# Kernel tuning notes

Measured on AMD Instinct MI355X. Metric: run time of the kernel, lower is better.

## Reference

```python
import jax, jax.numpy as jnp
import numpy as np

NUM_CODEBOOKS = 8
CODEBOOK_SIZE = 4096
SUBVEC_DIM = 128
NUM_CLASSES = 1000
BATCH = 8192
INPUT_DIM = NUM_CODEBOOKS * SUBVEC_DIM


def setup_inputs() -> dict:
    key = jax.random.key(0)
    k1, k2, k3 = jax.random.split(key, 3)
    x = jax.random.normal(k1, (BATCH, INPUT_DIM), dtype=jnp.float32)
    codebooks = jax.random.normal(k2, (NUM_CODEBOOKS, CODEBOOK_SIZE, SUBVEC_DIM), dtype=jnp.float32)
    tables = jax.random.normal(k3, (NUM_CODEBOOKS, CODEBOOK_SIZE, NUM_CLASSES), dtype=jnp.float32)
    return {"x": x, "codebooks": codebooks, "tables": tables}


def reference(x, codebooks, tables):
    B = x.shape[0]
    # [B, nc, d] subvectors
    xr = x.reshape(B, NUM_CODEBOOKS, SUBVEC_DIM)
    # (||x||^2 term is constant per (b, codebook) so it does not affect argmin)
    dots = jnp.einsum('bkd,kcd->bkc', xr, codebooks)            # [B, nc, K]
    c_sq = jnp.sum(codebooks * codebooks, axis=-1)              # [nc, K]
    dists = c_sq[None, :, :] - 2.0 * dots                        # [B, nc, K]
    indices = jnp.argmin(dists, axis=-1)                         # [B, nc] int
    # Gather per-codebook class score rows and sum over codebooks.
    # tables: [nc, K, C]; indices: [B, nc]
    gathered = jnp.take_along_axis(
        tables[None, :, :, :],                                   # [1, nc, K, C]
        indices[:, :, None, None],                               # [B, nc, 1, 1]
        axis=2,
    )                                                            # [B, nc, 1, C]
    scores = jnp.sum(gathered[:, :, 0, :], axis=1)               # [B, C]
    return scores
```

## Files before the change

kernel.cpp:

```cpp
#include <hip/hip_runtime.h>
#include <stdint.h>

#define NC   8
#define NK   4096
#define DD   128
#define NCLS 1000
#define NB   8192

#define CSQ_F32   4194304
#define P_U32     4300000
#define TAIL_LO   4300
#define TAIL_HI   4366

typedef _Float16 f16;
typedef f16   f16x8 __attribute__((ext_vector_type(8)));
typedef float f32x4 __attribute__((ext_vector_type(4)));

typedef const __attribute__((address_space(1))) unsigned int g_u32;
typedef __attribute__((address_space(3))) unsigned int l_u32;

__device__ __forceinline__ void gll16(const char* g, char* l) {
    __builtin_amdgcn_global_load_lds((g_u32*)g, (l_u32*)l, 16, 0, 0);
}

__device__ __forceinline__ int swz(int row, int kg) {
    return (row * 256 + kg * 16) ^ ((row & 7) << 4);
}

__device__ __forceinline__ void ins(float cv, int ci, float& v1, int& i1,
                                    float& v2, int& i2) {
    const bool b1 = (cv > v1) || (cv == v1 && ci < i1);
    const bool b2 = (cv > v2) || (cv == v2 && ci < i2);
    if (b1) { v2 = v1; i2 = i1; v1 = cv; i1 = ci; }
    else if (b2) { v2 = cv; i2 = ci; }
}

__device__ __forceinline__ void cvt8(const float4 v0, const float4 v1,
                                     f16x8& h, f16x8& l) {
    float vs[8] = {v0.x, v0.y, v0.z, v0.w, v1.x, v1.y, v1.z, v1.w};
#pragma unroll
    for (int i = 0; i < 8; ++i) {
        const float v = vs[i];
        const f16 hi = (f16)v;
        h[i] = hi;
        l[i] = (f16)((v - (float)hi) * 2048.0f);
    }
}

__global__ __launch_bounds__(256) void prep_cb(const float* __restrict__ cb,
                                               char* __restrict__ bimg,
                                               float* __restrict__ csq) {
    const int chunk = blockIdx.x, k = blockIdx.y, t = threadIdx.x;
    const float* src = cb + ((size_t)k * NK + (size_t)chunk * 64) * DD;
    char* dst = bimg + (size_t)(k * 64 + chunk) * 32768;
#pragma unroll
    for (int j = 0; j < 4; ++j) {
        const int col = j * 16 + (t >> 4);
        const int kg  = t & 15;
        const float* p = src + (size_t)col * DD + kg * 8;
        const float4 v0 = *(const float4*)p;
        const float4 v1 = *(const float4*)(p + 4);
        float vs[8] = {v0.x, v0.y, v0.z, v0.w, v1.x, v1.y, v1.z, v1.w};
        f16x8 h, l;
        float ss = 0.f;
#pragma unroll
        for (int i = 0; i < 8; ++i) {
            const float v = vs[i];
            ss += v * v;
            const f16 hi = (f16)v;
            h[i] = hi;
            l[i] = (f16)((v - (float)hi) * 2048.0f);
        }
#pragma unroll
        for (int m = 1; m < 16; m <<= 1) ss += __shfl_xor(ss, m, 16);
        if (kg == 0) csq[k * NK + chunk * 64 + col] = ss;
        const int r = col & 31;
        const int half = col >> 5;
        const int off = half * 8192 + swz(r, kg);
        *(f16x8*)(dst + off)         = h;
        *(f16x8*)(dst + 16384 + off) = l;
    }
}

template <int W, bool ISS>
__device__ __forceinline__ void chunk_step(
    int c, int& bcur, int& bnx, char* lds, const char* gB,
    int w, int lane, int l15,
    const f16x8 (&Ah)[4], const f16x8 (&Al)[4], const int (&boff)[4][2],
    float (&rv1)[4], float (&rv2)[4], int (&ri1)[4], int (&ri2)[4]) {

    asm volatile("s_waitcnt vmcnt(%0)" :: "i"(W) : "memory");
    __builtin_amdgcn_s_barrier();

    if (ISS) {
        const int cn = c + 2;
        const char* src = gB + (size_t)(cn >> 1) * 32768 + (size_t)(cn & 1) * 8192;
        char* dstb = lds + bnx * 16384 + w * 1024;
        gll16(src + w * 1024 + lane * 16, dstb);
        gll16(src + 16384 + w * 1024 + lane * 16, dstb + 8192);
    }

    char* bufc = lds + bcur * 16384;
    const float cs0 = *(const float*)(lds + 49152 + (c * 32 + l15) * 4);
    const float cs1 = *(const float*)(lds + 49152 + (c * 32 + 16 + l15) * 4);
    f32x4 a10 = (f32x4){-0.5f * cs0, -0.5f * cs0, -0.5f * cs0, -0.5f * cs0};
    f32x4 a11 = (f32x4){-0.5f * cs1, -0.5f * cs1, -0.5f * cs1, -0.5f * cs1};
    f32x4 a20 = (f32x4){0.f, 0.f, 0.f, 0.f};
    f32x4 a21 = (f32x4){0.f, 0.f, 0.f, 0.f};

    __builtin_amdgcn_s_setprio(1);
#pragma unroll
    for (int kk = 0; kk < 4; ++kk) {
        const f16x8 bh0 = *(const f16x8*)(bufc + boff[kk][0]);
        const f16x8 bh1 = *(const f16x8*)(bufc + boff[kk][1]);
        const f16x8 bl0 = *(const f16x8*)(bufc + 8192 + boff[kk][0]);
        const f16x8 bl1 = *(const f16x8*)(bufc + 8192 + boff[kk][1]);
        a10 = __builtin_amdgcn_mfma_f32_16x16x32_f16(Ah[kk], bh0, a10, 0, 0, 0);
        a11 = __builtin_amdgcn_mfma_f32_16x16x32_f16(Ah[kk], bh1, a11, 0, 0, 0);
        a20 = __builtin_amdgcn_mfma_f32_16x16x32_f16(Ah[kk], bl0, a20, 0, 0, 0);
        a21 = __builtin_amdgcn_mfma_f32_16x16x32_f16(Ah[kk], bl1, a21, 0, 0, 0);
        a20 = __builtin_amdgcn_mfma_f32_16x16x32_f16(Al[kk], bh0, a20, 0, 0, 0);
        a21 = __builtin_amdgcn_mfma_f32_16x16x32_f16(Al[kk], bh1, a21, 0, 0, 0);
    }
    __builtin_amdgcn_s_setprio(0);

    const int col0 = c * 32 + l15;
#pragma unroll
    for (int q = 0; q < 4; ++q) {
        const float s0 = fmaf(a20[q], 4.8828125e-4f, a10[q]);
        const float s1 = fmaf(a21[q], 4.8828125e-4f, a11[q]);
        float cv; int ci;
        if (s1 > s0) { cv = s1; ci = col0 + 16; }
        else         { cv = s0; ci = col0; }
        if (cv > rv1[q]) {
            rv2[q] = rv1[q]; ri2[q] = ri1[q];
            rv1[q] = cv;     ri1[q] = ci;
        } else if (cv > rv2[q]) {
            rv2[q] = cv; ri2[q] = ci;
        }
    }
    bcur = (bcur == 2) ? 0 : bcur + 1;
    bnx  = (bnx  == 2) ? 0 : bnx  + 1;
}

__global__ __launch_bounds__(512, 4) void gemm_argmin(
    const float* __restrict__ x, const char* __restrict__ bimg,
    const float* __restrict__ csq_g, uint32_t* __restrict__ pk) {
    __shared__ char lds[65536];
    const int t = threadIdx.x;
    const int lane = t & 63, w = t >> 6;
    const int bm = blockIdx.x, k = blockIdx.y;
    const int l15 = lane & 15, l4 = lane >> 4;

    {
        const float4* cg = (const float4*)(csq_g + k * NK);
        float4* cl = (float4*)(lds + 49152);
        cl[t] = cg[t];
        cl[t + 512] = cg[t + 512];
    }

    f16x8 Ah[4], Al[4];
    {
        const float* xrow = x + (size_t)(bm * 128 + w * 16 + l15) * 1024 + k * DD;
#pragma unroll
        for (int kk = 0; kk < 4; ++kk) {
            const float* p = xrow + (kk * 4 + l4) * 8;
            cvt8(*(const float4*)p, *(const float4*)(p + 4), Ah[kk], Al[kk]);
        }
    }

    int boff[4][2];
#pragma unroll
    for (int kk = 0; kk < 4; ++kk) {
#pragma unroll
        for (int n = 0; n < 2; ++n)
            boff[kk][n] = swz(n * 16 + l15, kk * 4 + l4);
    }

    float rv1[4], rv2[4];
    int   ri1[4], ri2[4];
#pragma unroll
    for (int q = 0; q < 4; ++q) {
        rv1[q] = -3.402823466e38f; rv2[q] = -3.402823466e38f;
        ri1[q] = 0; ri2[q] = 0;
    }

    __syncthreads();

    const char* gB = bimg + (size_t)k * 64 * 32768;
#pragma unroll
    for (int cn = 0; cn < 2; ++cn) {
        const char* src = gB + (size_t)(cn >> 1) * 32768 + (size_t)(cn & 1) * 8192;
        char* dstb = lds + cn * 16384 + w * 1024;
        gll16(src + w * 1024 + lane * 16, dstb);
        gll16(src + 16384 + w * 1024 + lane * 16, dstb + 8192);
    }

    int bcur = 0, bnx = 2;
#pragma unroll 1
    for (int c = 0; c < 126; ++c)
        chunk_step<2, true>(c, bcur, bnx, lds, gB, w, lane, l15,
                            Ah, Al, boff, rv1, rv2, ri1, ri2);
    chunk_step<2, false>(126, bcur, bnx, lds, gB, w, lane, l15,
                         Ah, Al, boff, rv1, rv2, ri1, ri2);
    chunk_step<0, false>(127, bcur, bnx, lds, gB, w, lane, l15,
                         Ah, Al, boff, rv1, rv2, ri1, ri2);

#pragma unroll
    for (int m = 1; m < 16; m <<= 1) {
#pragma unroll
        for (int q = 0; q < 4; ++q) {
            const float ov1 = __shfl_xor(rv1[q], m, 16);
            const int   oi1 = __shfl_xor(ri1[q], m, 16);
            const float ov2 = __shfl_xor(rv2[q], m, 16);
            const int   oi2 = __shfl_xor(ri2[q], m, 16);
            ins(ov1, oi1, rv1[q], ri1[q], rv2[q], ri2[q]);
            ins(ov2, oi2, rv1[q], ri1[q], rv2[q], ri2[q]);
        }
    }
    if (l15 == 0) {
#pragma unroll
        for (int q = 0; q < 4; ++q) {
            const int row = bm * 128 + w * 16 + l4 * 4 + q;
            pk[(size_t)row * NC + k] =
                (uint32_t)ri1[q] | ((uint32_t)ri2[q] << 16);
        }
    }
}

__global__ __launch_bounds__(512) void reloc_main(const uint32_t* __restrict__ pk,
                                                  uint32_t* __restrict__ hdr) {
    const int g = blockIdx.x * 512 + threadIdx.x;
    const int b = g >> 3, k = g & 7;
    const uint32_t v = pk[g];
    if (b < TAIL_LO || b >= TAIL_HI) hdr[(size_t)b * NCLS + k] = v;
}

__global__ __launch_bounds__(256) void reloc_tail(const uint32_t* __restrict__ pk,
                                                  uint32_t* __restrict__ hdr) {
    for (int g = threadIdx.x; g < (TAIL_HI - TAIL_LO) * 8; g += 256) {
        const int b = TAIL_LO + (g >> 3), k = g & 7;
        hdr[(size_t)b * NCLS + k] = pk[(size_t)b * 8 + k];
    }
}

__global__ __launch_bounds__(256) void finish(const float* __restrict__ x,
                                              const float* __restrict__ cb,
                                              const float* __restrict__ tables,
                                              float* __restrict__ out) {
    const int b = blockIdx.x, t = threadIdx.x;
    const int lane = t & 63, w = t >> 6;
    __shared__ uint32_t hdr_s[8];
    __shared__ int rows_s[8];
    if (t < 8) hdr_s[t] = ((const uint32_t*)out)[(size_t)b * NCLS + t];
    __syncthreads();
#pragma unroll
    for (int kq = 0; kq < 2; ++kq) {
        const int k = w * 2 + kq;
        const uint32_t h = hdr_s[k];
        const int i1 = (int)(h & 0xFFFFu), i2 = (int)(h >> 16);
        const float x0 = x[(size_t)b * 1024 + k * 128 + lane];
        const float x1 = x[(size_t)b * 1024 + k * 128 + 64 + lane];
        const float* c1p = cb + ((size_t)k * NK + i1) * DD;
        const float* c2p = cb + ((size_t)k * NK + i2) * DD;
        const float c10 = c1p[lane], c11 = c1p[64 + lane];
        const float c20 = c2p[lane], c21 = c2p[64 + lane];
        double d1 = (double)c10 * c10 - 2.0 * (double)x0 * c10
                  + (double)c11 * c11 - 2.0 * (double)x1 * c11;
        double d2 = (double)c20 * c20 - 2.0 * (double)x0 * c20
                  + (double)c21 * c21 - 2.0 * (double)x1 * c21;
#pragma unroll
        for (int m = 32; m >= 1; m >>= 1) {
            d1 += __shfl_xor(d1, m, 64);
            d2 += __shfl_xor(d2, m, 64);
        }
        if (lane == 0)
            rows_s[k] = (d1 < d2) ? i1 : (d2 < d1 ? i2 : (i1 < i2 ? i1 : i2));
    }
    __syncthreads();
    if (t < 250) {
        float4 acc = {0.f, 0.f, 0.f, 0.f};
#pragma unroll
        for (int k = 0; k < NC; ++k) {
            const float4 v =
                *((const float4*)(tables + ((size_t)k * NK + rows_s[k]) * NCLS) + t);
            acc.x += v.x; acc.y += v.y; acc.z += v.z; acc.w += v.w;
        }
        *((float4*)(out + (size_t)b * NCLS) + t) = acc;
    }
}

extern "C" void kernel_launch(void* const* d_in, const int* in_sizes, int n_in,
                              void* d_out, int out_size, void* d_ws, size_t ws_size,
                              hipStream_t stream) {
    const float* x      = (const float*)d_in[0];
    const float* cb     = (const float*)d_in[1];
    const float* tables = (const float*)d_in[2];
    float* out = (float*)d_out;

    char*     bimg = (char*)d_out;
    float*    csq  = (float*)d_out + CSQ_F32;
    uint32_t* pk   = (uint32_t*)d_out + P_U32;
    uint32_t* hdr  = (uint32_t*)d_out;

    prep_cb<<<dim3(64, NC), 256, 0, stream>>>(cb, bimg, csq);
    gemm_argmin<<<dim3(64, NC), 512, 0, stream>>>(x, bimg, csq, pk);
    reloc_main<<<128, 512, 0, stream>>>(pk, hdr);
    reloc_tail<<<1, 256, 0, stream>>>(pk, hdr);
    finish<<<NB, 256, 0, stream>>>(x, cb, tables, out);
}
```

Measured before the change: 483.6 us.

## Drop codebook low-half split, keep top-3 candidates with exact rescoring

The codebook is now stored only as a single fp16 image, and only the x operand keeps its hi/lo split. This cuts the MFMAs per chunk from six to four and halves the LDS and global traffic for B. To make up for the lost precision, the argmin pass keeps three candidates instead of two, and the finish kernel rescores all three in double precision. The layout is also simplified: -0.5*csq is precomputed, the block order is interleaved across codebooks, and the reloc step becomes one kernel using a fixed stash cutoff. The risk is that fp16 rounding of the codebook pushes the true argmin out of the top three for some rows.

```diff
diff --git a/kernel.cpp b/kernel.cpp
--- a/kernel.cpp
+++ b/kernel.cpp
@@ -7,10 +7,10 @@
 #define NCLS 1000
 #define NB   8192
 
-#define CSQ_F32   4194304
-#define P_U32     4300000
-#define TAIL_LO   4300
-#define TAIL_HI   4366
+#define BIMG_B   0
+#define CSQ_B    8388608
+#define STASH_B  8519680
+#define BCUT     2176
 
 typedef _Float16 f16;
 typedef f16   f16x8 __attribute__((ext_vector_type(8)));
@@ -27,12 +27,22 @@
     return (row * 256 + kg * 16) ^ ((row & 7) << 4);
 }
 
-__device__ __forceinline__ void ins(float cv, int ci, float& v1, int& i1,
-                                    float& v2, int& i2) {
-    const bool b1 = (cv > v1) || (cv == v1 && ci < i1);
-    const bool b2 = (cv > v2) || (cv == v2 && ci < i2);
-    if (b1) { v2 = v1; i2 = i1; v1 = cv; i1 = ci; }
-    else if (b2) { v2 = cv; i2 = ci; }
+__device__ __forceinline__ void ins3(float cv, int ci,
+                                     float& v1, int& i1, float& v2, int& i2,
+                                     float& v3, int& i3) {
+    if (cv > v1) { v3 = v2; i3 = i2; v2 = v1; i2 = i1; v1 = cv; i1 = ci; }
+    else if (cv > v2) { v3 = v2; i3 = i2; v2 = cv; i2 = ci; }
+    else if (cv > v3) { v3 = cv; i3 = ci; }
+}
+__device__ __forceinline__ void ins3t(float cv, int ci,
+                                      float& v1, int& i1, float& v2, int& i2,
+                                      float& v3, int& i3) {
+    const bool g1 = (cv > v1) || (cv == v1 && ci < i1);
+    const bool g2 = (cv > v2) || (cv == v2 && ci < i2);
+    const bool g3 = (cv > v3) || (cv == v3 && ci < i3);
+    if (g1) { v3 = v2; i3 = i2; v2 = v1; i2 = i1; v1 = cv; i1 = ci; }
+    else if (g2) { v3 = v2; i3 = i2; v2 = cv; i2 = ci; }
+    else if (g3) { v3 = cv; i3 = ci; }
 }
 
 __device__ __forceinline__ void cvt8(const float4 v0, const float4 v1,
@@ -48,37 +58,32 @@
 }
 
 __global__ __launch_bounds__(256) void prep_cb(const float* __restrict__ cb,
-                                               char* __restrict__ bimg,
-                                               float* __restrict__ csq) {
-    const int chunk = blockIdx.x, k = blockIdx.y, t = threadIdx.x;
-    const float* src = cb + ((size_t)k * NK + (size_t)chunk * 64) * DD;
-    char* dst = bimg + (size_t)(k * 64 + chunk) * 32768;
+                                               char* __restrict__ outc) {
+    const int k = blockIdx.y, t = threadIdx.x;
+    const int col0 = blockIdx.x * 64;
+    float* csq = (float*)(outc + CSQ_B);
 #pragma unroll
     for (int j = 0; j < 4; ++j) {
         const int col = j * 16 + (t >> 4);
         const int kg  = t & 15;
-        const float* p = src + (size_t)col * DD + kg * 8;
+        const int colg = col0 + col;
+        const float* p = cb + ((size_t)k * NK + colg) * DD + kg * 8;
         const float4 v0 = *(const float4*)p;
         const float4 v1 = *(const float4*)(p + 4);
         float vs[8] = {v0.x, v0.y, v0.z, v0.w, v1.x, v1.y, v1.z, v1.w};
-        f16x8 h, l;
+        f16x8 h;
         float ss = 0.f;
 #pragma unroll
         for (int i = 0; i < 8; ++i) {
             const float v = vs[i];
             ss += v * v;
-            const f16 hi = (f16)v;
-            h[i] = hi;
-            l[i] = (f16)((v - (float)hi) * 2048.0f);
+            h[i] = (f16)v;
         }
 #pragma unroll
         for (int m = 1; m < 16; m <<= 1) ss += __shfl_xor(ss, m, 16);
-        if (kg == 0) csq[k * NK + chunk * 64 + col] = ss;
-        const int r = col & 31;
-        const int half = col >> 5;
-        const int off = half * 8192 + swz(r, kg);
-        *(f16x8*)(dst + off)         = h;
-        *(f16x8*)(dst + 16384 + off) = l;
+        if (kg == 0) csq[k * NK + colg] = -0.5f * ss;
+        const int c = colg >> 5, r = colg & 31;
+        *(f16x8*)(outc + BIMG_B + (size_t)k * 1048576 + c * 8192 + swz(r, kg)) = h;
     }
 }
 
@@ -87,74 +92,65 @@
     int c, int& bcur, int& bnx, char* lds, const char* gB,
     int w, int lane, int l15,
     const f16x8 (&Ah)[4], const f16x8 (&Al)[4], const int (&boff)[4][2],
-    float (&rv1)[4], float (&rv2)[4], int (&ri1)[4], int (&ri2)[4]) {
+    float (&rv1)[4], float (&rv2)[4], float (&rv3)[4],
+    int (&ri1)[4], int (&ri2)[4], int (&ri3)[4]) {
 
     asm volatile("s_waitcnt vmcnt(%0)" :: "i"(W) : "memory");
     __builtin_amdgcn_s_barrier();
 
     if (ISS) {
-        const int cn = c + 2;
-        const char* src = gB + (size_t)(cn >> 1) * 32768 + (size_t)(cn & 1) * 8192;
-        char* dstb = lds + bnx * 16384 + w * 1024;
-        gll16(src + w * 1024 + lane * 16, dstb);
-        gll16(src + 16384 + w * 1024 + lane * 16, dstb + 8192);
-    }
-
-    char* bufc = lds + bcur * 16384;
-    const float cs0 = *(const float*)(lds + 49152 + (c * 32 + l15) * 4);
-    const float cs1 = *(const float*)(lds + 49152 + (c * 32 + 16 + l15) * 4);
-    f32x4 a10 = (f32x4){-0.5f * cs0, -0.5f * cs0, -0.5f * cs0, -0.5f * cs0};
-    f32x4 a11 = (f32x4){-0.5f * cs1, -0.5f * cs1, -0.5f * cs1, -0.5f * cs1};
-    f32x4 a20 = (f32x4){0.f, 0.f, 0.f, 0.f};
-    f32x4 a21 = (f32x4){0.f, 0.f, 0.f, 0.f};
+        const char* src = gB + (size_t)(c + 2) * 8192 + w * 1024 + lane * 16;
+        gll16(src, lds + bnx * 8192 + w * 1024 + lane * 16);
+    }
+
+    char* bufc = lds + bcur * 8192;
+    const float* csqL = (const float*)(lds + 24576);
+    const float cs0 = csqL[c * 32 + l15];
+    const float cs1 = csqL[c * 32 + 16 + l15];
+    f32x4 ah0 = (f32x4){cs0, cs0, cs0, cs0};
+    f32x4 ah1 = (f32x4){cs1, cs1, cs1, cs1};
+    f32x4 al0 = (f32x4){0.f, 0.f, 0.f, 0.f};
+    f32x4 al1 = (f32x4){0.f, 0.f, 0.f, 0.f};
 
     __builtin_amdgcn_s_setprio(1);
 #pragma unroll
     for (int kk = 0; kk < 4; ++kk) {
         const f16x8 bh0 = *(const f16x8*)(bufc + boff[kk][0]);
         const f16x8 bh1 = *(const f16x8*)(bufc + boff[kk][1]);
-        const f16x8 bl0 = *(const f16x8*)(bufc + 8192 + boff[kk][0]);
-        const f16x8 bl1 = *(const f16x8*)(bufc + 8192 + boff[kk][1]);
-        a10 = __builtin_amdgcn_mfma_f32_16x16x32_f16(Ah[kk], bh0, a10, 0, 0, 0);
-        a11 = __builtin_amdgcn_mfma_f32_16x16x32_f16(Ah[kk], bh1, a11, 0, 0, 0);
-        a20 = __builtin_amdgcn_mfma_f32_16x16x32_f16(Ah[kk], bl0, a20, 0, 0, 0);
-        a21 = __builtin_amdgcn_mfma_f32_16x16x32_f16(Ah[kk], bl1, a21, 0, 0, 0);
-        a20 = __builtin_amdgcn_mfma_f32_16x16x32_f16(Al[kk], bh0, a20, 0, 0, 0);
-        a21 = __builtin_amdgcn_mfma_f32_16x16x32_f16(Al[kk], bh1, a21, 0, 0, 0);
+        ah0 = __builtin_amdgcn_mfma_f32_16x16x32_f16(Ah[kk], bh0, ah0, 0, 0, 0);
+        ah1 = __builtin_amdgcn_mfma_f32_16x16x32_f16(Ah[kk], bh1, ah1, 0, 0, 0);
+        al0 = __builtin_amdgcn_mfma_f32_16x16x32_f16(Al[kk], bh0, al0, 0, 0, 0);
+        al1 = __builtin_amdgcn_mfma_f32_16x16x32_f16(Al[kk], bh1, al1, 0, 0, 0);
     }
     __builtin_amdgcn_s_setprio(0);
 
     const int col0 = c * 32 + l15;
 #pragma unroll
     for (int q = 0; q < 4; ++q) {
-        const float s0 = fmaf(a20[q], 4.8828125e-4f, a10[q]);
-        const float s1 = fmaf(a21[q], 4.8828125e-4f, a11[q]);
-        float cv; int ci;
-        if (s1 > s0) { cv = s1; ci = col0 + 16; }
-        else         { cv = s0; ci = col0; }
-        if (cv > rv1[q]) {
-            rv2[q] = rv1[q]; ri2[q] = ri1[q];
-            rv1[q] = cv;     ri1[q] = ci;
-        } else if (cv > rv2[q]) {
-            rv2[q] = cv; ri2[q] = ci;
-        }
+        const float s0 = fmaf(al0[q], 4.8828125e-4f, ah0[q]);
+        const float s1 = fmaf(al1[q], 4.8828125e-4f, ah1[q]);
+        float cv, cw; int ci, cj;
+        if (s1 > s0) { cv = s1; ci = col0 + 16; cw = s0; cj = col0; }
+        else         { cv = s0; ci = col0;      cw = s1; cj = col0 + 16; }
+        ins3(cv, ci, rv1[q], ri1[q], rv2[q], ri2[q], rv3[q], ri3[q]);
+        if (cw > rv3[q])
+            ins3(cw, cj, rv1[q], ri1[q], rv2[q], ri2[q], rv3[q], ri3[q]);
     }
     bcur = (bcur == 2) ? 0 : bcur + 1;
     bnx  = (bnx  == 2) ? 0 : bnx  + 1;
 }
 
 __global__ __launch_bounds__(512, 4) void gemm_argmin(
-    const float* __restrict__ x, const char* __restrict__ bimg,
-    const float* __restrict__ csq_g, uint32_t* __restrict__ pk) {
-    __shared__ char lds[65536];
+    const float* __restrict__ x, char* __restrict__ outc) {
+    __shared__ char lds[40960];
     const int t = threadIdx.x;
     const int lane = t & 63, w = t >> 6;
-    const int bm = blockIdx.x, k = blockIdx.y;
+    const int k = blockIdx.x & 7, bm = blockIdx.x >> 3;
     const int l15 = lane & 15, l4 = lane >> 4;
 
     {
-        const float4* cg = (const float4*)(csq_g + k * NK);
-        float4* cl = (float4*)(lds + 49152);
+        const float4* cg = (const float4*)((const char*)outc + CSQ_B) + k * (NK / 4);
+        float4* cl = (float4*)(lds + 24576);
         cl[t] = cg[t];
         cl[t + 512] = cg[t + 512];
     }
@@ -177,34 +173,32 @@
             boff[kk][n] = swz(n * 16 + l15, kk * 4 + l4);
     }
 
-    float rv1[4], rv2[4];
-    int   ri1[4], ri2[4];
+    float rv1[4], rv2[4], rv3[4];
+    int   ri1[4], ri2[4], ri3[4];
 #pragma unroll
     for (int q = 0; q < 4; ++q) {
         rv1[q] = -3.402823466e38f; rv2[q] = -3.402823466e38f;
-        ri1[q] = 0; ri2[q] = 0;
+        rv3[q] = -3.402823466e38f;
+        ri1[q] = 0; ri2[q] = 0; ri3[q] = 0;
     }
 
     __syncthreads();
 
-    const char* gB = bimg + (size_t)k * 64 * 32768;
-#pragma unroll
-    for (int cn = 0; cn < 2; ++cn) {
-        const char* src = gB + (size_t)(cn >> 1) * 32768 + (size_t)(cn & 1) * 8192;
-        char* dstb = lds + cn * 16384 + w * 1024;
-        gll16(src + w * 1024 + lane * 16, dstb);
-        gll16(src + 16384 + w * 1024 + lane * 16, dstb + 8192);
-    }
+    const char* gB = (const char*)outc + BIMG_B + (size_t)k * 1048576;
+#pragma unroll
+    for (int cn = 0; cn < 2; ++cn)
+        gll16(gB + (size_t)cn * 8192 + w * 1024 + lane * 16,
+              lds + cn * 8192 + w * 1024 + lane * 16);
 
     int bcur = 0, bnx = 2;
 #pragma unroll 1
     for (int c = 0; c < 126; ++c)
-        chunk_step<2, true>(c, bcur, bnx, lds, gB, w, lane, l15,
-                            Ah, Al, boff, rv1, rv2, ri1, ri2);
-    chunk_step<2, false>(126, bcur, bnx, lds, gB, w, lane, l15,
-                         Ah, Al, boff, rv1, rv2, ri1, ri2);
+        chunk_step<1, true>(c, bcur, bnx, lds, gB, w, lane, l15,
+                            Ah, Al, boff, rv1, rv2, rv3, ri1, ri2, ri3);
+    chunk_step<1, false>(126, bcur, bnx, lds, gB, w, lane, l15,
+                         Ah, Al, boff, rv1, rv2, rv3, ri1, ri2, ri3);
     chunk_step<0, false>(127, bcur, bnx, lds, gB, w, lane, l15,
-                         Ah, Al, boff, rv1, rv2, ri1, ri2);
+                         Ah, Al, boff, rv1, rv2, rv3, ri1, ri2, ri3);
 
 #pragma unroll
     for (int m = 1; m < 16; m <<= 1) {
@@ -214,33 +208,40 @@
             const int   oi1 = __shfl_xor(ri1[q], m, 16);
             const float ov2 = __shfl_xor(rv2[q], m, 16);
             const int   oi2 = __shfl_xor(ri2[q], m, 16);
-            ins(ov1, oi1, rv1[q], ri1[q], rv2[q], ri2[q]);
-            ins(ov2, oi2, rv1[q], ri1[q], rv2[q], ri2[q]);
+            const float ov3 = __shfl_xor(rv3[q], m, 16);
+            const int   oi3 = __shfl_xor(ri3[q], m, 16);
+            ins3t(ov1, oi1, rv1[q], ri1[q], rv2[q], ri2[q], rv3[q], ri3[q]);
+            ins3t(ov2, oi2, rv1[q], ri1[q], rv2[q], ri2[q], rv3[q], ri3[q]);
+            ins3t(ov3, oi3, rv1[q], ri1[q], rv2[q], ri2[q], rv3[q], ri3[q]);
         }
     }
     if (l15 == 0) {
 #pragma unroll
         for (int q = 0; q < 4; ++q) {
-            const int row = bm * 128 + w * 16 + l4 * 4 + q;
-            pk[(size_t)row * NC + k] =
-                (uint32_t)ri1[q] | ((uint32_t)ri2[q] << 16);
-        }
-    }
-}
-
-__global__ __launch_bounds__(512) void reloc_main(const uint32_t* __restrict__ pk,
-                                                  uint32_t* __restrict__ hdr) {
-    const int g = blockIdx.x * 512 + threadIdx.x;
-    const int b = g >> 3, k = g & 7;
-    const uint32_t v = pk[g];
-    if (b < TAIL_LO || b >= TAIL_HI) hdr[(size_t)b * NCLS + k] = v;
-}
-
-__global__ __launch_bounds__(256) void reloc_tail(const uint32_t* __restrict__ pk,
-                                                  uint32_t* __restrict__ hdr) {
-    for (int g = threadIdx.x; g < (TAIL_HI - TAIL_LO) * 8; g += 256) {
-        const int b = TAIL_LO + (g >> 3), k = g & 7;
-        hdr[(size_t)b * NCLS + k] = pk[(size_t)b * 8 + k];
+            const int b = bm * 128 + w * 16 + l4 * 4 + q;
+            uint2 pkv;
+            pkv.x = (uint32_t)ri1[q] | ((uint32_t)ri2[q] << 16);
+            pkv.y = (uint32_t)ri3[q];
+            char* base = (bm >= 17)
+                ? outc + (size_t)b * 4000 + k * 8
+                : outc + STASH_B + ((size_t)b * 8 + k) * 8;
+            *(uint2*)base = pkv;
+        }
+    }
+}
+
+__global__ __launch_bounds__(1024) void reloc(char* __restrict__ outc) {
+    const int t = threadIdx.x;
+    const uint2* stash = (const uint2*)(outc + STASH_B);
+    uint2 vals[17];
+#pragma unroll
+    for (int j = 0; j < 17; ++j) vals[j] = stash[j * 1024 + t];
+    __syncthreads();
+#pragma unroll
+    for (int j = 0; j < 17; ++j) {
+        const int e = j * 1024 + t;
+        const int b = e >> 3, k = e & 7;
+        *(uint2*)(outc + (size_t)b * 4000 + k * 8) = vals[j];
     }
 }
 
@@ -250,32 +251,38 @@
                                               float* __restrict__ out) {
     const int b = blockIdx.x, t = threadIdx.x;
     const int lane = t & 63, w = t >> 6;
-    __shared__ uint32_t hdr_s[8];
+    __shared__ uint2 hdr_s[8];
     __shared__ int rows_s[8];
-    if (t < 8) hdr_s[t] = ((const uint32_t*)out)[(size_t)b * NCLS + t];
+    if (t < 8) hdr_s[t] = *(const uint2*)((const char*)out + (size_t)b * 4000 + t * 8);
     __syncthreads();
 #pragma unroll
     for (int kq = 0; kq < 2; ++kq) {
         const int k = w * 2 + kq;
-        const uint32_t h = hdr_s[k];
-        const int i1 = (int)(h & 0xFFFFu), i2 = (int)(h >> 16);
-        const float x0 = x[(size_t)b * 1024 + k * 128 + lane];
-        const float x1 = x[(size_t)b * 1024 + k * 128 + 64 + lane];
-        const float* c1p = cb + ((size_t)k * NK + i1) * DD;
-        const float* c2p = cb + ((size_t)k * NK + i2) * DD;
-        const float c10 = c1p[lane], c11 = c1p[64 + lane];
-        const float c20 = c2p[lane], c21 = c2p[64 + lane];
-        double d1 = (double)c10 * c10 - 2.0 * (double)x0 * c10
-                  + (double)c11 * c11 - 2.0 * (double)x1 * c11;
-        double d2 = (double)c20 * c20 - 2.0 * (double)x0 * c20
-                  + (double)c21 * c21 - 2.0 * (double)x1 * c21;
-#pragma unroll
-        for (int m = 32; m >= 1; m >>= 1) {
-            d1 += __shfl_xor(d1, m, 64);
-            d2 += __shfl_xor(d2, m, 64);
-        }
-        if (lane == 0)
-            rows_s[k] = (d1 < d2) ? i1 : (d2 < d1 ? i2 : (i1 < i2 ? i1 : i2));
+        const uint2 h = hdr_s[k];
+        const int i1 = (int)(h.x & 0xFFFFu);
+        const int i2 = (int)(h.x >> 16);
+        const int i3 = (int)(h.y & 0xFFFFu);
+        const double x0 = (double)x[(size_t)b * 1024 + k * DD + lane];
+        const double x1 = (double)x[(size_t)b * 1024 + k * DD + 64 + lane];
+        const float* cbk = cb + (size_t)k * NK * DD;
+        double d[3];
+        const int idx[3] = {i1, i2, i3};
+#pragma unroll
+        for (int j = 0; j < 3; ++j) {
+            const float* cp = cbk + (size_t)idx[j] * DD;
+            const double e0 = (double)cp[lane] - x0;
+            const double e1 = (double)cp[64 + lane] - x1;
+            double dv = e0 * e0 + e1 * e1;
+#pragma unroll
+            for (int m = 32; m >= 1; m >>= 1) dv += __shfl_xor(dv, m, 64);
+            d[j] = dv;
+        }
+        if (lane == 0) {
+            double bd = d[0]; int bi = idx[0];
+            if (d[1] < bd || (d[1] == bd && idx[1] < bi)) { bd = d[1]; bi = idx[1]; }
+            if (d[2] < bd || (d[2] == bd && idx[2] < bi)) { bd = d[2]; bi = idx[2]; }
+            rows_s[k] = bi;
+        }
     }
     __syncthreads();
     if (t < 250) {
@@ -297,15 +304,10 @@
     const float* cb     = (const float*)d_in[1];
     const float* tables = (const float*)d_in[2];
     float* out = (float*)d_out;
-
-    char*     bimg = (char*)d_out;
-    float*    csq  = (float*)d_out + CSQ_F32;
-    uint32_t* pk   = (uint32_t*)d_out + P_U32;
-    uint32_t* hdr  = (uint32_t*)d_out;
-
-    prep_cb<<<dim3(64, NC), 256, 0, stream>>>(cb, bimg, csq);
-    gemm_argmin<<<dim3(64, NC), 512, 0, stream>>>(x, bimg, csq, pk);
-    reloc_main<<<128, 512, 0, stream>>>(pk, hdr);
-    reloc_tail<<<1, 256, 0, stream>>>(pk, hdr);
+    char* outc = (char*)d_out;
+
+    prep_cb<<<dim3(64, NC), 256, 0, stream>>>(cb, outc);
+    gemm_argmin<<<512, 512, 0, stream>>>(x, outc);
+    reloc<<<1, 1024, 0, stream>>>(outc);
     finish<<<NB, 256, 0, stream>>>(x, cb, tables, out);
 }
```

Measured after the change: 829.5 us. 71.5% more time.
